# Kernel tuning notes

Measured on AMD Instinct MI355X. Metric: run time of the kernel, lower is better.

The kernel has to match this reference:

```python
import jax, jax.numpy as jnp
import numpy as np

B, M, D = 2048, 8192, 2048
SIM_THRESH = 0.5   # hard similarity cutoff (sims > 0.5)
ALPHA = 0.5        # dynamic threshold = mean - ALPHA * std
EPS = 1e-8         # torch cosine_similarity eps
NEG = -1e9         # masked-out logit for softmax


def setup_inputs() -> dict:
    key = jax.random.key(0)
    k1, k2, k3, k4 = jax.random.split(key, 4)
    query = jax.random.normal(k1, (B, D), jnp.float32)
    # Correlate memory bank with queries so cosine sims exceed the 0.5 threshold
    # for ~M/B entries per query (matched pairs have sim ~ 1/sqrt(1+0.75^2) ~ 0.8).
    idx = jax.random.randint(k2, (M,), 0, B)
    noise = jax.random.normal(k3, (M, D), jnp.float32)
    query_set = query[idx] + 0.75 * noise
    target_set = jax.random.normal(k4, (M, D), jnp.float32)
    return {"query": query, "query_set": query_set, "target_set": target_set}


def reference(query, query_set, target_set):
    # --- cosine similarity: [B, M] ---
    qn = query / jnp.maximum(jnp.linalg.norm(query, axis=-1, keepdims=True), EPS)
    sn = query_set / jnp.maximum(jnp.linalg.norm(query_set, axis=-1, keepdims=True), EPS)
    sims = jnp.einsum("bd,md->bm", qn, sn)  # [B, M]

    # --- first hard mask ---
    mask = sims > SIM_THRESH                              # [B, M]
    cnt = mask.sum(axis=-1)                               # [B]
    safe_cnt = jnp.maximum(cnt, 1).astype(sims.dtype)
    mean = jnp.where(mask, sims, 0.0).sum(-1) / safe_cnt  # masked mean  [B]
    var = (jnp.where(mask, (sims - mean[:, None]) ** 2, 0.0).sum(-1) / safe_cnt)
    std = jnp.sqrt(var)                                   # population std (unbiased=False)

    # --- dynamic threshold re-mask ---
    dyn_thr = mean - ALPHA * std                          # [B]
    final_mask = mask & (sims > dyn_thr[:, None])         # [B, M]
    fcnt = final_mask.sum(axis=-1)                        # [B]

    # --- softmax-weighted gather over surviving entries ---
    logits = jnp.where(final_mask, sims, NEG)
    w = jax.nn.softmax(logits, axis=-1)
    w = jnp.where(final_mask, w, 0.0)
    weighted = jnp.einsum("bm,md->bd", w, target_set)     # [B, D]

    # --- fallback 1: final mask empty -> target at argmin |sim - mean| ---
    closest = jnp.argmin(jnp.abs(sims - mean[:, None]), axis=-1)  # [B]
    fallback = target_set[closest]                        # [B, D]
    out = jnp.where((fcnt > 0)[:, None], weighted, fallback)

    # --- fallback 2: first mask empty -> zeros ---
    out = jnp.where((cnt > 0)[:, None], out, 0.0)
    return out
```

## Files before the change

kernel.cpp:

```cpp
#include <hip/hip_runtime.h>
#include <hip/hip_bf16.h>
#include <hip/hip_fp8.h>

#define B_DIM 2048
#define M_DIM 8192
#define D_DIM 2048
#define EPSN 1e-8f
#define ALPHA_C 0.5f
#define SIM_T 0.5f
#define SCREEN_T 0.35f
#define CAP 2048

typedef __attribute__((ext_vector_type(4))) float f32x4;
typedef __attribute__((ext_vector_type(16))) float f32x16;

__global__ __launch_bounds__(256) void prep_kernel(const float* __restrict__ q,
                                                   const float* __restrict__ s,
                                                   unsigned char* __restrict__ A8,
                                                   unsigned char* __restrict__ B8,
                                                   float* __restrict__ rq,
                                                   float* __restrict__ rs,
                                                   int* __restrict__ ccnt) {
    const int row = blockIdx.x;
    const int tid = threadIdx.x;
    const float* src;
    unsigned char* dst;
    float* rdst;
    if (row < B_DIM) {
        src = q + (size_t)row * D_DIM; dst = A8 + (size_t)row * D_DIM; rdst = rq + row;
        if (tid == 0) ccnt[row] = 0;
    } else {
        int r = row - B_DIM;
        src = s + (size_t)r * D_DIM; dst = B8 + (size_t)r * D_DIM; rdst = rs + r;
    }
    const float4* src4 = (const float4*)src;
    float4 v0 = src4[2 * tid];
    float4 v1 = src4[2 * tid + 1];
    float acc = v0.x * v0.x + v0.y * v0.y + v0.z * v0.z + v0.w * v0.w
              + v1.x * v1.x + v1.y * v1.y + v1.z * v1.z + v1.w * v1.w;
    #pragma unroll
    for (int o = 32; o > 0; o >>= 1) acc += __shfl_down(acc, o, 64);
    __shared__ float red[4];
    if ((tid & 63) == 0) red[tid >> 6] = acc;
    __syncthreads();
    const float tot = red[0] + red[1] + red[2] + red[3];
    const float scale = 1.0f / fmaxf(sqrtf(tot), EPSN);
    if (tid == 0) *rdst = scale;

    float xs[8] = {v0.x * scale, v0.y * scale, v0.z * scale, v0.w * scale,
                   v1.x * scale, v1.y * scale, v1.z * scale, v1.w * scale};
#if __has_builtin(__builtin_amdgcn_cvt_pk_fp8_f32)
    int w0 = __builtin_amdgcn_cvt_pk_fp8_f32(xs[0], xs[1], 0, false);
    w0     = __builtin_amdgcn_cvt_pk_fp8_f32(xs[2], xs[3], w0, true);
    int w1 = __builtin_amdgcn_cvt_pk_fp8_f32(xs[4], xs[5], 0, false);
    w1     = __builtin_amdgcn_cvt_pk_fp8_f32(xs[6], xs[7], w1, true);
    uint2 u;
    u.x = (unsigned)w0;
    u.y = (unsigned)w1;
    ((uint2*)dst)[tid] = u;
#else
    union { unsigned char b[8]; uint2 u; } pk;
    #pragma unroll
    for (int e = 0; e < 8; e++) {
        __hip_fp8_e4m3 f(xs[e]);
        pk.b[e] = f.__x;
    }
    ((uint2*)dst)[tid] = pk.u;
#endif
}

#define BKC 64
#define NCHUNK (D_DIM / BKC)
#define SLOT_SZ 32768

#define GLOAD_LDS16(g, l) \
    __builtin_amdgcn_global_load_lds((const __attribute__((address_space(1))) void*)(g), \
                                     (__attribute__((address_space(3))) void*)(l), 16, 0, 0)

#define STAGE(jj, l) GLOAD_LDS16(gsrc[l] + (size_t)(jj) * BKC, \
                                 lds + (((jj) & 3) * SLOT_SZ) + ldsDst[l])

__global__ __launch_bounds__(512, 2) void gemm_screen(const unsigned char* __restrict__ A8,
                                                      const unsigned char* __restrict__ B8,
                                                      int* __restrict__ ccnt,
                                                      int* __restrict__ cidx) {
    extern __shared__ unsigned char lds[];

    const int tid = threadIdx.x;
    const int wave = tid >> 6;
    const int lane = tid & 63;
    const int row0 = blockIdx.y * 256;
    const int col0 = blockIdx.x * 256;
    const int wm = (wave >> 2) * 128;
    const int wn = (wave & 3) * 64;

    f32x16 acc[4][2];
    #pragma unroll
    for (int i = 0; i < 4; i++)
        #pragma unroll
        for (int j = 0; j < 2; j++)
            #pragma unroll
            for (int r = 0; r < 16; r++) acc[i][j][r] = 0.f;

    const int Lr = lane >> 2;
    const int scn = (lane & 3) ^ ((lane >> 3) & 3);
    const unsigned char* gsrc[4];
    int ldsDst[4];
    #pragma unroll
    for (int l = 0; l < 4; l++) {
        const int r = (l & 1) * 128 + wave * 16 + Lr;
        const unsigned char* base = (l >> 1) ? (B8 + (size_t)(col0 + r) * D_DIM)
                                             : (A8 + (size_t)(row0 + r) * D_DIM);
        gsrc[l] = base + scn * 16;
        ldsDst[l] = (l >> 1) * 16384 + ((l & 1) * 128 + wave * 16) * 64;
    }

    const int r31 = lane & 31;
    const int hi8 = (lane >> 5) * 8;
    const int swz = (r31 >> 1) & 3;

    #pragma unroll
    for (int j = 0; j < 3; j++) {
        STAGE(j, 0); STAGE(j, 1); STAGE(j, 2); STAGE(j, 3);
    }

    for (int j = 0; j < NCHUNK; j++) {
        if (j < NCHUNK - 2)       asm volatile("s_waitcnt vmcnt(8)" ::: "memory");
        else if (j == NCHUNK - 2) asm volatile("s_waitcnt vmcnt(4)" ::: "memory");
        else                      asm volatile("s_waitcnt vmcnt(0)" ::: "memory");
        __builtin_amdgcn_s_barrier();

        const unsigned char* sb = lds + (j & 3) * SLOT_SZ;
        const int js = j + 3;

        #pragma unroll
        for (int t = 0; t < 4; t++) {
            const int off = ((t ^ swz) * 16) + hi8;
            long afr[4], bfr[2];
            #pragma unroll
            for (int nj = 0; nj < 2; nj++)
                bfr[nj] = *(const long*)(sb + 16384 + (wn + nj * 32 + r31) * 64 + off);
            #pragma unroll
            for (int i = 0; i < 4; i++)
                afr[i] = *(const long*)(sb + (wm + i * 32 + r31) * 64 + off);
            if (js < NCHUNK) STAGE(js, t);
            __builtin_amdgcn_s_setprio(1);
            #pragma unroll
            for (int i = 0; i < 4; i++)
                #pragma unroll
                for (int nj = 0; nj < 2; nj++)
                    acc[i][nj] = __builtin_amdgcn_mfma_f32_32x32x16_fp8_fp8(
                        afr[i], bfr[nj], acc[i][nj], 0, 0, 0);
            __builtin_amdgcn_s_setprio(0);
        }
    }

    #pragma unroll
    for (int nj = 0; nj < 2; nj++) {
        const int col = col0 + wn + nj * 32 + r31;
        #pragma unroll
        for (int i = 0; i < 4; i++) {
            const int rbase = row0 + wm + i * 32 + (hi8 >> 1);
            #pragma unroll
            for (int r = 0; r < 16; r++) {
                if (acc[i][nj][r] > SCREEN_T) {
                    const int row = rbase + (r & 3) + 8 * (r >> 2);
                    int pos = atomicAdd(&ccnt[row], 1);
                    if (pos < CAP) cidx[(size_t)row * CAP + pos] = col;
                }
            }
        }
    }
}

__device__ inline float wred_sum(float v) {
    #pragma unroll
    for (int o = 32; o > 0; o >>= 1) v += __shfl_down(v, o, 64);
    return v;
}
__device__ inline float wred_max(float v) {
    #pragma unroll
    for (int o = 32; o > 0; o >>= 1) v = fmaxf(v, __shfl_down(v, o, 64));
    return v;
}
__device__ inline int wred_sumi(int v) {
    #pragma unroll
    for (int o = 32; o > 0; o >>= 1) v += __shfl_down(v, o, 64);
    return v;
}
__device__ inline unsigned long long wred_minu64(unsigned long long v) {
    #pragma unroll
    for (int o = 32; o > 0; o >>= 1) {
        unsigned long long w = __shfl_down(v, o, 64);
        v = (w < v) ? w : v;
    }
    return v;
}

__global__ __launch_bounds__(256) void stats_gather(const float* __restrict__ q,
                                                    const float* __restrict__ s,
                                                    const float* __restrict__ T,
                                                    const float* __restrict__ rq,
                                                    const float* __restrict__ rs,
                                                    const int* __restrict__ ccnt,
                                                    const int* __restrict__ cidx,
                                                    float* __restrict__ out) {
    const int b = blockIdx.x;
    const int tid = threadIdx.x;
    const int lane = tid & 63, wave = tid >> 6;
    __shared__ float qrow[D_DIM];
    __shared__ float cval[CAP];
    __shared__ float rf[4], rg[4];
    __shared__ int ri[4];
    __shared__ unsigned long long ru[4];

    const int nc = min(ccnt[b], CAP);
    const float qscale = rq[b];

    {
        const float4* q4 = (const float4*)(q + (size_t)b * D_DIM);
        float4 v0 = q4[tid], v1 = q4[tid + 256];
        v0.x *= qscale; v0.y *= qscale; v0.z *= qscale; v0.w *= qscale;
        v1.x *= qscale; v1.y *= qscale; v1.z *= qscale; v1.w *= qscale;
        ((float4*)qrow)[tid] = v0;
        ((float4*)qrow)[tid + 256] = v1;
    }
    __syncthreads();

    const int* myidx = cidx + (size_t)b * CAP;
    for (int k = wave; k < nc; k += 4) {
        const int m = myidx[k];
        const float4* s4 = (const float4*)(s + (size_t)m * D_DIM);
        const float4* q4 = (const float4*)qrow;
        float p = 0.f;
        #pragma unroll
        for (int e = 0; e < 8; e++) {
            float4 sv = s4[lane + e * 64];
            float4 qv = q4[lane + e * 64];
            p = fmaf(sv.x, qv.x, p); p = fmaf(sv.y, qv.y, p);
            p = fmaf(sv.z, qv.z, p); p = fmaf(sv.w, qv.w, p);
        }
        p = wred_sum(p);
        if (lane == 0) cval[k] = p * rs[m];
    }
    __syncthreads();

    float psum = 0.f, pmax = -1e30f;
    int pcnt = 0;
    for (int k = tid; k < nc; k += 256) {
        float v = cval[k];
        if (v > SIM_T) { pcnt++; psum += v; pmax = fmaxf(pmax, v); }
    }
    psum = wred_sum(psum); pmax = wred_max(pmax); pcnt = wred_sumi(pcnt);
    if (lane == 0) { rf[wave] = psum; rg[wave] = pmax; ri[wave] = pcnt; }
    __syncthreads();
    const int cnt = ri[0] + ri[1] + ri[2] + ri[3];
    const float mean = (rf[0] + rf[1] + rf[2] + rf[3]) / (float)max(cnt, 1);
    const float mx = fmaxf(fmaxf(rg[0], rg[1]), fmaxf(rg[2], rg[3]));
    __syncthreads();

    float pvar = 0.f;
    unsigned long long pkey = 0xffffffffffffffffull;
    for (int k = tid; k < nc; k += 256) {
        float v = cval[k];
        if (v > SIM_T) { float d = v - mean; pvar += d * d; }
        unsigned long long kk = ((unsigned long long)__float_as_uint(fabsf(v - mean)) << 32)
                              | (unsigned)myidx[k];
        pkey = (kk < pkey) ? kk : pkey;
    }
    pvar = wred_sum(pvar); pkey = wred_minu64(pkey);
    if (lane == 0) { rf[wave] = pvar; ru[wave] = pkey; }
    __syncthreads();
    const float var = (rf[0] + rf[1] + rf[2] + rf[3]) / (float)max(cnt, 1);
    const float dyn = mean - ALPHA_C * sqrtf(var);
    unsigned long long k0 = ru[0] < ru[1] ? ru[0] : ru[1];
    unsigned long long k1 = ru[2] < ru[3] ? ru[2] : ru[3];
    const int closest = (int)(unsigned)((k0 < k1 ? k0 : k1) & 0xffffffffull);
    __syncthreads();

    float pden = 0.f;
    int pf = 0;
    for (int k = tid; k < nc; k += 256) {
        float v = cval[k];
        if (v > SIM_T && v > dyn) { pden += expf(v - mx); pf++; }
    }
    pden = wred_sum(pden); pf = wred_sumi(pf);
    if (lane == 0) { rf[wave] = pden; ri[wave] = pf; }
    __syncthreads();
    const float denom = rf[0] + rf[1] + rf[2] + rf[3];
    const int fcnt = ri[0] + ri[1] + ri[2] + ri[3];

    const float4* T4 = (const float4*)T;
    float4 a0 = make_float4(0.f, 0.f, 0.f, 0.f);
    float4 a1 = make_float4(0.f, 0.f, 0.f, 0.f);
    if (cnt == 0) {
    } else if (fcnt == 0) {
        a0 = T4[(size_t)closest * (D_DIM / 4) + tid];
        a1 = T4[(size_t)closest * (D_DIM / 4) + tid + 256];
    } else {
        const float rden = 1.0f / denom;
        for (int k = 0; k < nc; k++) {
            float v = cval[k];
            if (v > SIM_T && v > dyn) {
                const int m = myidx[k];
                const float w = expf(v - mx) * rden;
                float4 t0 = T4[(size_t)m * (D_DIM / 4) + tid];
                float4 t1 = T4[(size_t)m * (D_DIM / 4) + tid + 256];
                a0.x += w * t0.x; a0.y += w * t0.y; a0.z += w * t0.z; a0.w += w * t0.w;
                a1.x += w * t1.x; a1.y += w * t1.y; a1.z += w * t1.z; a1.w += w * t1.w;
            }
        }
    }
    float4* out4 = (float4*)(out + (size_t)b * D_DIM);
    out4[tid] = a0;
    out4[tid + 256] = a1;
}

extern "C" void kernel_launch(void* const* d_in, const int* in_sizes, int n_in,
                              void* d_out, int out_size, void* d_ws, size_t ws_size,
                              hipStream_t stream) {
    const float* query = (const float*)d_in[0];
    const float* qset  = (const float*)d_in[1];
    const float* tset  = (const float*)d_in[2];
    float* out = (float*)d_out;

    char* ws = (char*)d_ws;
    size_t off = 0;
    unsigned char* A8 = (unsigned char*)(ws + off); off += (size_t)B_DIM * D_DIM;
    unsigned char* B8 = (unsigned char*)(ws + off); off += (size_t)M_DIM * D_DIM;
    float* rq   = (float*)(ws + off);  off += B_DIM * sizeof(float);
    float* rs   = (float*)(ws + off);  off += M_DIM * sizeof(float);
    int* ccnt   = (int*)(ws + off);    off += B_DIM * sizeof(int);
    int* cidx   = (int*)(ws + off);    off += (size_t)B_DIM * CAP * sizeof(int);

    hipLaunchKernelGGL(prep_kernel, dim3(B_DIM + M_DIM), dim3(256), 0, stream,
                       query, qset, A8, B8, rq, rs, ccnt);
    hipLaunchKernelGGL(gemm_screen, dim3(M_DIM / 256, B_DIM / 256), dim3(512), 131072, stream,
                       A8, B8, ccnt, cidx);
    hipLaunchKernelGGL(stats_gather, dim3(B_DIM), dim3(256), 0, stream,
                       query, qset, tset, rq, rs, ccnt, cidx, out);
}
```

Measured before the change: 228.1 us.

## Fuse prep, screening GEMM and gather into one cooperative persistent kernel

Merges the three launches (normalize/quantize prep, FP8 screening GEMM, per-query stats and gather) into a single cooperative kernel. Two grid-wide syncs separate the phases. The grid is 256 blocks of 512 threads, and each block loops over queries in the final phase. This removes inter-kernel launch gaps and the prep kernel's separate tail. In exchange, the latency-bound gather phase now runs with far fewer resident waves, since each block keeps about 147KB of LDS, and the grid barriers add their own cost.

```diff
diff --git a/kernel.cpp b/kernel.cpp
--- a/kernel.cpp
+++ b/kernel.cpp
@@ -1,6 +1,9 @@
 #include <hip/hip_runtime.h>
+#include <hip/hip_cooperative_groups.h>
 #include <hip/hip_bf16.h>
 #include <hip/hip_fp8.h>
+
+namespace cg = cooperative_groups;
 
 #define B_DIM 2048
 #define M_DIM 8192
@@ -14,61 +17,6 @@
 typedef __attribute__((ext_vector_type(4))) float f32x4;
 typedef __attribute__((ext_vector_type(16))) float f32x16;
 
-__global__ __launch_bounds__(256) void prep_kernel(const float* __restrict__ q,
-                                                   const float* __restrict__ s,
-                                                   unsigned char* __restrict__ A8,
-                                                   unsigned char* __restrict__ B8,
-                                                   float* __restrict__ rq,
-                                                   float* __restrict__ rs,
-                                                   int* __restrict__ ccnt) {
-    const int row = blockIdx.x;
-    const int tid = threadIdx.x;
-    const float* src;
-    unsigned char* dst;
-    float* rdst;
-    if (row < B_DIM) {
-        src = q + (size_t)row * D_DIM; dst = A8 + (size_t)row * D_DIM; rdst = rq + row;
-        if (tid == 0) ccnt[row] = 0;
-    } else {
-        int r = row - B_DIM;
-        src = s + (size_t)r * D_DIM; dst = B8 + (size_t)r * D_DIM; rdst = rs + r;
-    }
-    const float4* src4 = (const float4*)src;
-    float4 v0 = src4[2 * tid];
-    float4 v1 = src4[2 * tid + 1];
-    float acc = v0.x * v0.x + v0.y * v0.y + v0.z * v0.z + v0.w * v0.w
-              + v1.x * v1.x + v1.y * v1.y + v1.z * v1.z + v1.w * v1.w;
-    #pragma unroll
-    for (int o = 32; o > 0; o >>= 1) acc += __shfl_down(acc, o, 64);
-    __shared__ float red[4];
-    if ((tid & 63) == 0) red[tid >> 6] = acc;
-    __syncthreads();
-    const float tot = red[0] + red[1] + red[2] + red[3];
-    const float scale = 1.0f / fmaxf(sqrtf(tot), EPSN);
-    if (tid == 0) *rdst = scale;
-
-    float xs[8] = {v0.x * scale, v0.y * scale, v0.z * scale, v0.w * scale,
-                   v1.x * scale, v1.y * scale, v1.z * scale, v1.w * scale};
-#if __has_builtin(__builtin_amdgcn_cvt_pk_fp8_f32)
-    int w0 = __builtin_amdgcn_cvt_pk_fp8_f32(xs[0], xs[1], 0, false);
-    w0     = __builtin_amdgcn_cvt_pk_fp8_f32(xs[2], xs[3], w0, true);
-    int w1 = __builtin_amdgcn_cvt_pk_fp8_f32(xs[4], xs[5], 0, false);
-    w1     = __builtin_amdgcn_cvt_pk_fp8_f32(xs[6], xs[7], w1, true);
-    uint2 u;
-    u.x = (unsigned)w0;
-    u.y = (unsigned)w1;
-    ((uint2*)dst)[tid] = u;
-#else
-    union { unsigned char b[8]; uint2 u; } pk;
-    #pragma unroll
-    for (int e = 0; e < 8; e++) {
-        __hip_fp8_e4m3 f(xs[e]);
-        pk.b[e] = f.__x;
-    }
-    ((uint2*)dst)[tid] = pk.u;
-#endif
-}
-
 #define BKC 64
 #define NCHUNK (D_DIM / BKC)
 #define SLOT_SZ 32768
@@ -79,99 +27,6 @@
 
 #define STAGE(jj, l) GLOAD_LDS16(gsrc[l] + (size_t)(jj) * BKC, \
                                  lds + (((jj) & 3) * SLOT_SZ) + ldsDst[l])
-
-__global__ __launch_bounds__(512, 2) void gemm_screen(const unsigned char* __restrict__ A8,
-                                                      const unsigned char* __restrict__ B8,
-                                                      int* __restrict__ ccnt,
-                                                      int* __restrict__ cidx) {
-    extern __shared__ unsigned char lds[];
-
-    const int tid = threadIdx.x;
-    const int wave = tid >> 6;
-    const int lane = tid & 63;
-    const int row0 = blockIdx.y * 256;
-    const int col0 = blockIdx.x * 256;
-    const int wm = (wave >> 2) * 128;
-    const int wn = (wave & 3) * 64;
-
-    f32x16 acc[4][2];
-    #pragma unroll
-    for (int i = 0; i < 4; i++)
-        #pragma unroll
-        for (int j = 0; j < 2; j++)
-            #pragma unroll
-            for (int r = 0; r < 16; r++) acc[i][j][r] = 0.f;
-
-    const int Lr = lane >> 2;
-    const int scn = (lane & 3) ^ ((lane >> 3) & 3);
-    const unsigned char* gsrc[4];
-    int ldsDst[4];
-    #pragma unroll
-    for (int l = 0; l < 4; l++) {
-        const int r = (l & 1) * 128 + wave * 16 + Lr;
-        const unsigned char* base = (l >> 1) ? (B8 + (size_t)(col0 + r) * D_DIM)
-                                             : (A8 + (size_t)(row0 + r) * D_DIM);
-        gsrc[l] = base + scn * 16;
-        ldsDst[l] = (l >> 1) * 16384 + ((l & 1) * 128 + wave * 16) * 64;
-    }
-
-    const int r31 = lane & 31;
-    const int hi8 = (lane >> 5) * 8;
-    const int swz = (r31 >> 1) & 3;
-
-    #pragma unroll
-    for (int j = 0; j < 3; j++) {
-        STAGE(j, 0); STAGE(j, 1); STAGE(j, 2); STAGE(j, 3);
-    }
-
-    for (int j = 0; j < NCHUNK; j++) {
-        if (j < NCHUNK - 2)       asm volatile("s_waitcnt vmcnt(8)" ::: "memory");
-        else if (j == NCHUNK - 2) asm volatile("s_waitcnt vmcnt(4)" ::: "memory");
-        else                      asm volatile("s_waitcnt vmcnt(0)" ::: "memory");
-        __builtin_amdgcn_s_barrier();
-
-        const unsigned char* sb = lds + (j & 3) * SLOT_SZ;
-        const int js = j + 3;
-
-        #pragma unroll
-        for (int t = 0; t < 4; t++) {
-            const int off = ((t ^ swz) * 16) + hi8;
-            long afr[4], bfr[2];
-            #pragma unroll
-            for (int nj = 0; nj < 2; nj++)
-                bfr[nj] = *(const long*)(sb + 16384 + (wn + nj * 32 + r31) * 64 + off);
-            #pragma unroll
-            for (int i = 0; i < 4; i++)
-                afr[i] = *(const long*)(sb + (wm + i * 32 + r31) * 64 + off);
-            if (js < NCHUNK) STAGE(js, t);
-            __builtin_amdgcn_s_setprio(1);
-            #pragma unroll
-            for (int i = 0; i < 4; i++)
-                #pragma unroll
-                for (int nj = 0; nj < 2; nj++)
-                    acc[i][nj] = __builtin_amdgcn_mfma_f32_32x32x16_fp8_fp8(
-                        afr[i], bfr[nj], acc[i][nj], 0, 0, 0);
-            __builtin_amdgcn_s_setprio(0);
-        }
-    }
-
-    #pragma unroll
-    for (int nj = 0; nj < 2; nj++) {
-        const int col = col0 + wn + nj * 32 + r31;
-        #pragma unroll
-        for (int i = 0; i < 4; i++) {
-            const int rbase = row0 + wm + i * 32 + (hi8 >> 1);
-            #pragma unroll
-            for (int r = 0; r < 16; r++) {
-                if (acc[i][nj][r] > SCREEN_T) {
-                    const int row = rbase + (r & 3) + 8 * (r >> 2);
-                    int pos = atomicAdd(&ccnt[row], 1);
-                    if (pos < CAP) cidx[(size_t)row * CAP + pos] = col;
-                }
-            }
-        }
-    }
-}
 
 __device__ inline float wred_sum(float v) {
     #pragma unroll
@@ -197,123 +52,257 @@
     return v;
 }
 
-__global__ __launch_bounds__(256) void stats_gather(const float* __restrict__ q,
+__global__ __launch_bounds__(512, 2) void fused_all(const float* __restrict__ q,
                                                     const float* __restrict__ s,
                                                     const float* __restrict__ T,
-                                                    const float* __restrict__ rq,
-                                                    const float* __restrict__ rs,
-                                                    const int* __restrict__ ccnt,
-                                                    const int* __restrict__ cidx,
+                                                    unsigned char* __restrict__ A8,
+                                                    unsigned char* __restrict__ B8,
+                                                    float* __restrict__ rq,
+                                                    float* __restrict__ rs,
+                                                    int* __restrict__ ccnt,
+                                                    int* __restrict__ cidx,
                                                     float* __restrict__ out) {
-    const int b = blockIdx.x;
-    const int tid = threadIdx.x;
-    const int lane = tid & 63, wave = tid >> 6;
+    extern __shared__ unsigned char lds[];
     __shared__ float qrow[D_DIM];
     __shared__ float cval[CAP];
-    __shared__ float rf[4], rg[4];
-    __shared__ int ri[4];
-    __shared__ unsigned long long ru[4];
-
-    const int nc = min(ccnt[b], CAP);
-    const float qscale = rq[b];
+    __shared__ float rf[8], rg[8];
+    __shared__ int ri[8];
+    __shared__ unsigned long long ru[8];
+
+    const int tid = threadIdx.x;
+    const int wave = tid >> 6;
+    const int lane = tid & 63;
+    const int blk = blockIdx.x;
 
     {
-        const float4* q4 = (const float4*)(q + (size_t)b * D_DIM);
-        float4 v0 = q4[tid], v1 = q4[tid + 256];
-        v0.x *= qscale; v0.y *= qscale; v0.z *= qscale; v0.w *= qscale;
-        v1.x *= qscale; v1.y *= qscale; v1.z *= qscale; v1.w *= qscale;
-        ((float4*)qrow)[tid] = v0;
-        ((float4*)qrow)[tid + 256] = v1;
+        const int worker = blk * 8 + wave;
+        for (int it = 0; it < 5; ++it) {
+            const int r = worker + it * 2048;
+            const float* src = (r < B_DIM) ? q + (size_t)r * D_DIM
+                                           : s + (size_t)(r - B_DIM) * D_DIM;
+            const float4* s4 = (const float4*)src;
+            float4 v[8];
+            float acc = 0.f;
+            #pragma unroll
+            for (int e = 0; e < 8; ++e) {
+                v[e] = s4[lane + e * 64];
+                acc += v[e].x * v[e].x + v[e].y * v[e].y
+                     + v[e].z * v[e].z + v[e].w * v[e].w;
+            }
+            #pragma unroll
+            for (int o = 32; o > 0; o >>= 1) acc += __shfl_xor(acc, o, 64);
+            const float scale = 1.0f / fmaxf(sqrtf(acc), EPSN);
+            unsigned int* dst = (r < B_DIM)
+                ? (unsigned int*)(A8 + (size_t)r * D_DIM)
+                : (unsigned int*)(B8 + (size_t)(r - B_DIM) * D_DIM);
+            if (lane == 0) {
+                if (r < B_DIM) { rq[r] = scale; ccnt[r] = 0; }
+                else           { rs[r - B_DIM] = scale; }
+            }
+            #pragma unroll
+            for (int e = 0; e < 8; ++e) {
+#if __has_builtin(__builtin_amdgcn_cvt_pk_fp8_f32)
+                int w0 = __builtin_amdgcn_cvt_pk_fp8_f32(v[e].x * scale, v[e].y * scale, 0, false);
+                w0     = __builtin_amdgcn_cvt_pk_fp8_f32(v[e].z * scale, v[e].w * scale, w0, true);
+                dst[lane + e * 64] = (unsigned)w0;
+#else
+                union { unsigned char b[4]; unsigned u; } pk;
+                float xs[4] = {v[e].x * scale, v[e].y * scale, v[e].z * scale, v[e].w * scale};
+                #pragma unroll
+                for (int c = 0; c < 4; c++) { __hip_fp8_e4m3 f(xs[c]); pk.b[c] = f.__x; }
+                dst[lane + e * 64] = pk.u;
+#endif
+            }
+        }
     }
-    __syncthreads();
-
-    const int* myidx = cidx + (size_t)b * CAP;
-    for (int k = wave; k < nc; k += 4) {
-        const int m = myidx[k];
-        const float4* s4 = (const float4*)(s + (size_t)m * D_DIM);
-        const float4* q4 = (const float4*)qrow;
-        float p = 0.f;
-        #pragma unroll
-        for (int e = 0; e < 8; e++) {
-            float4 sv = s4[lane + e * 64];
-            float4 qv = q4[lane + e * 64];
-            p = fmaf(sv.x, qv.x, p); p = fmaf(sv.y, qv.y, p);
-            p = fmaf(sv.z, qv.z, p); p = fmaf(sv.w, qv.w, p);
-        }
-        p = wred_sum(p);
-        if (lane == 0) cval[k] = p * rs[m];
+    cg::this_grid().sync();
+
+    {
+        const int col0 = (blk & 31) * 256;
+        const int row0 = (blk >> 5) * 256;
+        const int wm = (wave >> 2) * 128;
+        const int wn = (wave & 3) * 64;
+
+        f32x16 acc[4][2];
+        #pragma unroll
+        for (int i = 0; i < 4; i++)
+            #pragma unroll
+            for (int j = 0; j < 2; j++)
+                #pragma unroll
+                for (int r = 0; r < 16; r++) acc[i][j][r] = 0.f;
+
+        const int Lr = lane >> 2;
+        const int scn = (lane & 3) ^ ((lane >> 3) & 3);
+        const unsigned char* gsrc[4];
+        int ldsDst[4];
+        #pragma unroll
+        for (int l = 0; l < 4; l++) {
+            const int r = (l & 1) * 128 + wave * 16 + Lr;
+            const unsigned char* base = (l >> 1) ? (B8 + (size_t)(col0 + r) * D_DIM)
+                                                 : (A8 + (size_t)(row0 + r) * D_DIM);
+            gsrc[l] = base + scn * 16;
+            ldsDst[l] = (l >> 1) * 16384 + ((l & 1) * 128 + wave * 16) * 64;
+        }
+
+        const int r31 = lane & 31;
+        const int hi8 = (lane >> 5) * 8;
+        const int swz = (r31 >> 1) & 3;
+
+        #pragma unroll
+        for (int j = 0; j < 3; j++) {
+            STAGE(j, 0); STAGE(j, 1); STAGE(j, 2); STAGE(j, 3);
+        }
+
+        for (int j = 0; j < NCHUNK; j++) {
+            if (j < NCHUNK - 2)       asm volatile("s_waitcnt vmcnt(8)" ::: "memory");
+            else if (j == NCHUNK - 2) asm volatile("s_waitcnt vmcnt(4)" ::: "memory");
+            else                      asm volatile("s_waitcnt vmcnt(0)" ::: "memory");
+            __builtin_amdgcn_s_barrier();
+
+            const unsigned char* sb = lds + (j & 3) * SLOT_SZ;
+            const int js = j + 3;
+
+            #pragma unroll
+            for (int t = 0; t < 4; t++) {
+                const int off = ((t ^ swz) * 16) + hi8;
+                long afr[4], bfr[2];
+                #pragma unroll
+                for (int nj = 0; nj < 2; nj++)
+                    bfr[nj] = *(const long*)(sb + 16384 + (wn + nj * 32 + r31) * 64 + off);
+                #pragma unroll
+                for (int i = 0; i < 4; i++)
+                    afr[i] = *(const long*)(sb + (wm + i * 32 + r31) * 64 + off);
+                if (js < NCHUNK) STAGE(js, t);
+                __builtin_amdgcn_s_setprio(1);
+                #pragma unroll
+                for (int i = 0; i < 4; i++)
+                    #pragma unroll
+                    for (int nj = 0; nj < 2; nj++)
+                        acc[i][nj] = __builtin_amdgcn_mfma_f32_32x32x16_fp8_fp8(
+                            afr[i], bfr[nj], acc[i][nj], 0, 0, 0);
+                __builtin_amdgcn_s_setprio(0);
+            }
+        }
+
+        #pragma unroll
+        for (int nj = 0; nj < 2; nj++) {
+            const int col = col0 + wn + nj * 32 + r31;
+            #pragma unroll
+            for (int i = 0; i < 4; i++) {
+                const int rbase = row0 + wm + i * 32 + (hi8 >> 1);
+                #pragma unroll
+                for (int r = 0; r < 16; r++) {
+                    if (acc[i][nj][r] > SCREEN_T) {
+                        const int row = rbase + (r & 3) + 8 * (r >> 2);
+                        int pos = atomicAdd(&ccnt[row], 1);
+                        if (pos < CAP) cidx[(size_t)row * CAP + pos] = col;
+                    }
+                }
+            }
+        }
     }
-    __syncthreads();
-
-    float psum = 0.f, pmax = -1e30f;
-    int pcnt = 0;
-    for (int k = tid; k < nc; k += 256) {
-        float v = cval[k];
-        if (v > SIM_T) { pcnt++; psum += v; pmax = fmaxf(pmax, v); }
+    cg::this_grid().sync();
+
+    for (int bq = blk; bq < B_DIM; bq += 256) {
+        __syncthreads();
+        const int nc = min(ccnt[bq], CAP);
+        const float qscale = rq[bq];
+
+        {
+            const float4* q4 = (const float4*)(q + (size_t)bq * D_DIM);
+            float4 v0 = q4[tid];
+            v0.x *= qscale; v0.y *= qscale; v0.z *= qscale; v0.w *= qscale;
+            ((float4*)qrow)[tid] = v0;
+        }
+        __syncthreads();
+
+        const int* myidx = cidx + (size_t)bq * CAP;
+        for (int k = wave; k < nc; k += 8) {
+            const int m = myidx[k];
+            const float4* s4 = (const float4*)(s + (size_t)m * D_DIM);
+            const float4* q4 = (const float4*)qrow;
+            float p = 0.f;
+            #pragma unroll
+            for (int e = 0; e < 8; e++) {
+                float4 sv = s4[lane + e * 64];
+                float4 qv = q4[lane + e * 64];
+                p = fmaf(sv.x, qv.x, p); p = fmaf(sv.y, qv.y, p);
+                p = fmaf(sv.z, qv.z, p); p = fmaf(sv.w, qv.w, p);
+            }
+            p = wred_sum(p);
+            if (lane == 0) cval[k] = p * rs[m];
+        }
+        __syncthreads();
+
+        float psum = 0.f, pmax = -1e30f;
+        int pcnt = 0;
+        for (int k = tid; k < nc; k += 512) {
+            float v = cval[k];
+            if (v > SIM_T) { pcnt++; psum += v; pmax = fmaxf(pmax, v); }
+        }
+        psum = wred_sum(psum); pmax = wred_max(pmax); pcnt = wred_sumi(pcnt);
+        if (lane == 0) { rf[wave] = psum; rg[wave] = pmax; ri[wave] = pcnt; }
+        __syncthreads();
+        int cnt = 0; float msum = 0.f, mx = -1e30f;
+        #pragma unroll
+        for (int w = 0; w < 8; ++w) { cnt += ri[w]; msum += rf[w]; mx = fmaxf(mx, rg[w]); }
+        const float mean = msum / (float)max(cnt, 1);
+        __syncthreads();
+
+        float pvar = 0.f;
+        unsigned long long pkey = 0xffffffffffffffffull;
+        for (int k = tid; k < nc; k += 512) {
+            float v = cval[k];
+            if (v > SIM_T) { float d = v - mean; pvar += d * d; }
+            unsigned long long kk = ((unsigned long long)__float_as_uint(fabsf(v - mean)) << 32)
+                                  | (unsigned)myidx[k];
+            pkey = (kk < pkey) ? kk : pkey;
+        }
+        pvar = wred_sum(pvar); pkey = wred_minu64(pkey);
+        if (lane == 0) { rf[wave] = pvar; ru[wave] = pkey; }
+        __syncthreads();
+        float vsum = 0.f;
+        unsigned long long kmin = 0xffffffffffffffffull;
+        #pragma unroll
+        for (int w = 0; w < 8; ++w) { vsum += rf[w]; kmin = (ru[w] < kmin) ? ru[w] : kmin; }
+        const float var = vsum / (float)max(cnt, 1);
+        const float dyn = mean - ALPHA_C * sqrtf(var);
+        const int closest = (int)(unsigned)(kmin & 0xffffffffull);
+        __syncthreads();
+
+        float pden = 0.f;
+        int pf = 0;
+        for (int k = tid; k < nc; k += 512) {
+            float v = cval[k];
+            if (v > SIM_T && v > dyn) { pden += expf(v - mx); pf++; }
+        }
+        pden = wred_sum(pden); pf = wred_sumi(pf);
+        if (lane == 0) { rf[wave] = pden; ri[wave] = pf; }
+        __syncthreads();
+        float denom = 0.f; int fcnt = 0;
+        #pragma unroll
+        for (int w = 0; w < 8; ++w) { denom += rf[w]; fcnt += ri[w]; }
+
+        const float4* T4 = (const float4*)T;
+        float4 a0 = make_float4(0.f, 0.f, 0.f, 0.f);
+        if (cnt == 0) {
+        } else if (fcnt == 0) {
+            a0 = T4[(size_t)closest * (D_DIM / 4) + tid];
+        } else {
+            const float rden = 1.0f / denom;
+            for (int k = 0; k < nc; k++) {
+                float v = cval[k];
+                if (v > SIM_T && v > dyn) {
+                    const int m = myidx[k];
+                    const float w = expf(v - mx) * rden;
+                    float4 t0 = T4[(size_t)m * (D_DIM / 4) + tid];
+                    a0.x += w * t0.x; a0.y += w * t0.y;
+                    a0.z += w * t0.z; a0.w += w * t0.w;
+                }
+            }
+        }
+        ((float4*)(out + (size_t)bq * D_DIM))[tid] = a0;
     }
-    psum = wred_sum(psum); pmax = wred_max(pmax); pcnt = wred_sumi(pcnt);
-    if (lane == 0) { rf[wave] = psum; rg[wave] = pmax; ri[wave] = pcnt; }
-    __syncthreads();
-    const int cnt = ri[0] + ri[1] + ri[2] + ri[3];
-    const float mean = (rf[0] + rf[1] + rf[2] + rf[3]) / (float)max(cnt, 1);
-    const float mx = fmaxf(fmaxf(rg[0], rg[1]), fmaxf(rg[2], rg[3]));
-    __syncthreads();
-
-    float pvar = 0.f;
-    unsigned long long pkey = 0xffffffffffffffffull;
-    for (int k = tid; k < nc; k += 256) {
-        float v = cval[k];
-        if (v > SIM_T) { float d = v - mean; pvar += d * d; }
-        unsigned long long kk = ((unsigned long long)__float_as_uint(fabsf(v - mean)) << 32)
-                              | (unsigned)myidx[k];
-        pkey = (kk < pkey) ? kk : pkey;
-    }
-    pvar = wred_sum(pvar); pkey = wred_minu64(pkey);
-    if (lane == 0) { rf[wave] = pvar; ru[wave] = pkey; }
-    __syncthreads();
-    const float var = (rf[0] + rf[1] + rf[2] + rf[3]) / (float)max(cnt, 1);
-    const float dyn = mean - ALPHA_C * sqrtf(var);
-    unsigned long long k0 = ru[0] < ru[1] ? ru[0] : ru[1];
-    unsigned long long k1 = ru[2] < ru[3] ? ru[2] : ru[3];
-    const int closest = (int)(unsigned)((k0 < k1 ? k0 : k1) & 0xffffffffull);
-    __syncthreads();
-
-    float pden = 0.f;
-    int pf = 0;
-    for (int k = tid; k < nc; k += 256) {
-        float v = cval[k];
-        if (v > SIM_T && v > dyn) { pden += expf(v - mx); pf++; }
-    }
-    pden = wred_sum(pden); pf = wred_sumi(pf);
-    if (lane == 0) { rf[wave] = pden; ri[wave] = pf; }
-    __syncthreads();
-    const float denom = rf[0] + rf[1] + rf[2] + rf[3];
-    const int fcnt = ri[0] + ri[1] + ri[2] + ri[3];
-
-    const float4* T4 = (const float4*)T;
-    float4 a0 = make_float4(0.f, 0.f, 0.f, 0.f);
-    float4 a1 = make_float4(0.f, 0.f, 0.f, 0.f);
-    if (cnt == 0) {
-    } else if (fcnt == 0) {
-        a0 = T4[(size_t)closest * (D_DIM / 4) + tid];
-        a1 = T4[(size_t)closest * (D_DIM / 4) + tid + 256];
-    } else {
-        const float rden = 1.0f / denom;
-        for (int k = 0; k < nc; k++) {
-            float v = cval[k];
-            if (v > SIM_T && v > dyn) {
-                const int m = myidx[k];
-                const float w = expf(v - mx) * rden;
-                float4 t0 = T4[(size_t)m * (D_DIM / 4) + tid];
-                float4 t1 = T4[(size_t)m * (D_DIM / 4) + tid + 256];
-                a0.x += w * t0.x; a0.y += w * t0.y; a0.z += w * t0.z; a0.w += w * t0.w;
-                a1.x += w * t1.x; a1.y += w * t1.y; a1.z += w * t1.z; a1.w += w * t1.w;
-            }
-        }
-    }
-    float4* out4 = (float4*)(out + (size_t)b * D_DIM);
-    out4[tid] = a0;
-    out4[tid + 256] = a1;
 }
 
 extern "C" void kernel_launch(void* const* d_in, const int* in_sizes, int n_in,
@@ -333,10 +322,9 @@
     int* ccnt   = (int*)(ws + off);    off += B_DIM * sizeof(int);
     int* cidx   = (int*)(ws + off);    off += (size_t)B_DIM * CAP * sizeof(int);
 
-    hipLaunchKernelGGL(prep_kernel, dim3(B_DIM + M_DIM), dim3(256), 0, stream,
-                       query, qset, A8, B8, rq, rs, ccnt);
-    hipLaunchKernelGGL(gemm_screen, dim3(M_DIM / 256, B_DIM / 256), dim3(512), 131072, stream,
-                       A8, B8, ccnt, cidx);
-    hipLaunchKernelGGL(stats_gather, dim3(B_DIM), dim3(256), 0, stream,
-                       query, qset, tset, rq, rs, ccnt, cidx, out);
-}
+    void* args[] = {(void*)&query, (void*)&qset, (void*)&tset,
+                    (void*)&A8, (void*)&B8, (void*)&rq, (void*)&rs,
+                    (void*)&ccnt, (void*)&cidx, (void*)&out};
+    hipLaunchCooperativeKernel((const void*)fused_all, dim3(256), dim3(512),
+                               args, 131072, stream);
+}
```

Result: slower. 337.4 us (+47.9%).

## Shrink screening GEMM tile to 128x256 with 4 waves and double buffering

Applied to the files above, without the earlier changes.

Changes the FP8 screening GEMM from 256x256 tiles with 8 waves and a 4-slot LDS ring to 128x256 tiles with 4 waves, 2x4 MFMA per wave, and a 2-slot LDS buffer of 48KB. The grid doubles to 512 blocks for better CU fill, and the lower LDS use allows more blocks per CU. In exchange it waits for all loads (vmcnt(0)) each chunk, so prefetch depth drops to one chunk. Per-block data reuse is also lower.

```diff
diff --git a/kernel.cpp b/kernel.cpp
--- a/kernel.cpp
+++ b/kernel.cpp
@@ -69,50 +69,59 @@
 #endif
 }
 
+#define BM 128
+#define BN 256
 #define BKC 64
 #define NCHUNK (D_DIM / BKC)
-#define SLOT_SZ 32768
+#define SLOT_SZ ((BM + BN) * BKC)
+#define NLOADS 6
 
 #define GLOAD_LDS16(g, l) \
     __builtin_amdgcn_global_load_lds((const __attribute__((address_space(1))) void*)(g), \
                                      (__attribute__((address_space(3))) void*)(l), 16, 0, 0)
 
 #define STAGE(jj, l) GLOAD_LDS16(gsrc[l] + (size_t)(jj) * BKC, \
-                                 lds + (((jj) & 3) * SLOT_SZ) + ldsDst[l])
-
-__global__ __launch_bounds__(512, 2) void gemm_screen(const unsigned char* __restrict__ A8,
-                                                      const unsigned char* __restrict__ B8,
-                                                      int* __restrict__ ccnt,
-                                                      int* __restrict__ cidx) {
+                                 lds + (((jj) & 1) * SLOT_SZ) + ldsDst[l])
+
+__global__ __launch_bounds__(256) void gemm_screen(const unsigned char* __restrict__ A8,
+                                                   const unsigned char* __restrict__ B8,
+                                                   int* __restrict__ ccnt,
+                                                   int* __restrict__ cidx) {
     extern __shared__ unsigned char lds[];
 
     const int tid = threadIdx.x;
     const int wave = tid >> 6;
     const int lane = tid & 63;
-    const int row0 = blockIdx.y * 256;
-    const int col0 = blockIdx.x * 256;
-    const int wm = (wave >> 2) * 128;
-    const int wn = (wave & 3) * 64;
-
-    f32x16 acc[4][2];
-    #pragma unroll
-    for (int i = 0; i < 4; i++)
+    const int row0 = blockIdx.y * BM;
+    const int col0 = blockIdx.x * BN;
+    const int wm = (wave >> 1) * 64;
+    const int wn = (wave & 1) * 128;
+
+    f32x16 acc[2][4];
+    #pragma unroll
+    for (int i = 0; i < 2; i++)
         #pragma unroll
-        for (int j = 0; j < 2; j++)
+        for (int j = 0; j < 4; j++)
             #pragma unroll
             for (int r = 0; r < 16; r++) acc[i][j][r] = 0.f;
 
     const int Lr = lane >> 2;
     const int scn = (lane & 3) ^ ((lane >> 3) & 3);
-    const unsigned char* gsrc[4];
-    int ldsDst[4];
-    #pragma unroll
-    for (int l = 0; l < 4; l++) {
-        const int r = (l & 1) * 128 + wave * 16 + Lr;
-        const unsigned char* base = (l >> 1) ? (B8 + (size_t)(col0 + r) * D_DIM)
-                                             : (A8 + (size_t)(row0 + r) * D_DIM);
-        gsrc[l] = base + scn * 16;
-        ldsDst[l] = (l >> 1) * 16384 + ((l & 1) * 128 + wave * 16) * 64;
+    const unsigned char* gsrc[NLOADS];
+    int ldsDst[NLOADS];
+    #pragma unroll
+    for (int l = 0; l < NLOADS; l++) {
+        int trow, ldsOff;
+        if (l < 2) {
+            trow = wave * 32 + l * 16;
+            ldsOff = trow * 64;
+            gsrc[l] = A8 + (size_t)(row0 + trow + Lr) * D_DIM + scn * 16;
+        } else {
+            trow = wave * 64 + (l - 2) * 16;
+            ldsOff = BM * 64 + trow * 64;
+            gsrc[l] = B8 + (size_t)(col0 + trow + Lr) * D_DIM + scn * 16;
+        }
+        ldsDst[l] = ldsOff;
     }
 
     const int r31 = lane & 31;
@@ -120,35 +129,37 @@
     const int swz = (r31 >> 1) & 3;
 
     #pragma unroll
-    for (int j = 0; j < 3; j++) {
-        STAGE(j, 0); STAGE(j, 1); STAGE(j, 2); STAGE(j, 3);
-    }
+    for (int l = 0; l < NLOADS; l++) STAGE(0, l);
 
     for (int j = 0; j < NCHUNK; j++) {
-        if (j < NCHUNK - 2)       asm volatile("s_waitcnt vmcnt(8)" ::: "memory");
-        else if (j == NCHUNK - 2) asm volatile("s_waitcnt vmcnt(4)" ::: "memory");
-        else                      asm volatile("s_waitcnt vmcnt(0)" ::: "memory");
+        asm volatile("s_waitcnt vmcnt(0)" ::: "memory");
         __builtin_amdgcn_s_barrier();
 
-        const unsigned char* sb = lds + (j & 3) * SLOT_SZ;
-        const int js = j + 3;
+        const unsigned char* sb = lds + (j & 1) * SLOT_SZ;
+        const unsigned char* sbB = sb + BM * 64;
+        const int js = j + 1;
 
         #pragma unroll
         for (int t = 0; t < 4; t++) {
             const int off = ((t ^ swz) * 16) + hi8;
-            long afr[4], bfr[2];
-            #pragma unroll
-            for (int nj = 0; nj < 2; nj++)
-                bfr[nj] = *(const long*)(sb + 16384 + (wn + nj * 32 + r31) * 64 + off);
-            #pragma unroll
-            for (int i = 0; i < 4; i++)
+            long afr[2], bfr[4];
+            #pragma unroll
+            for (int nj = 0; nj < 4; nj++)
+                bfr[nj] = *(const long*)(sbB + (wn + nj * 32 + r31) * 64 + off);
+            #pragma unroll
+            for (int i = 0; i < 2; i++)
                 afr[i] = *(const long*)(sb + (wm + i * 32 + r31) * 64 + off);
-            if (js < NCHUNK) STAGE(js, t);
+            if (js < NCHUNK) {
+                if (t == 0)      { STAGE(js, 0); STAGE(js, 1); }
+                else if (t == 1) { STAGE(js, 2); STAGE(js, 3); }
+                else if (t == 2) { STAGE(js, 4); }
+                else             { STAGE(js, 5); }
+            }
             __builtin_amdgcn_s_setprio(1);
             #pragma unroll
-            for (int i = 0; i < 4; i++)
+            for (int i = 0; i < 2; i++)
                 #pragma unroll
-                for (int nj = 0; nj < 2; nj++)
+                for (int nj = 0; nj < 4; nj++)
                     acc[i][nj] = __builtin_amdgcn_mfma_f32_32x32x16_fp8_fp8(
                         afr[i], bfr[nj], acc[i][nj], 0, 0, 0);
             __builtin_amdgcn_s_setprio(0);
@@ -156,10 +167,10 @@
     }
 
     #pragma unroll
-    for (int nj = 0; nj < 2; nj++) {
+    for (int nj = 0; nj < 4; nj++) {
         const int col = col0 + wn + nj * 32 + r31;
         #pragma unroll
-        for (int i = 0; i < 4; i++) {
+        for (int i = 0; i < 2; i++) {
             const int rbase = row0 + wm + i * 32 + (hi8 >> 1);
             #pragma unroll
             for (int r = 0; r < 16; r++) {
@@ -335,7 +346,7 @@
 
     hipLaunchKernelGGL(prep_kernel, dim3(B_DIM + M_DIM), dim3(256), 0, stream,
                        query, qset, A8, B8, rq, rs, ccnt);
-    hipLaunchKernelGGL(gemm_screen, dim3(M_DIM / 256, B_DIM / 256), dim3(512), 131072, stream,
+    hipLaunchKernelGGL(gemm_screen, dim3(M_DIM / BN, B_DIM / BM), dim3(256), 49152, stream,
                        A8, B8, ccnt, cidx);
     hipLaunchKernelGGL(stats_gather, dim3(B_DIM), dim3(256), 0, stream,
                        query, qset, tset, rq, rs, ccnt, cidx, out);
```

After: 228.6 us. No clear change (+0.2%).
